# Kernel optimization log

Hardware: AMD Instinct MI355X
Metric: run time of the kernel (lower is better)

Reference implementation:

```python
import jax, jax.numpy as jnp
import numpy as np

N = 40000    # nodes
E = 500000   # edges
B = 512      # graphs
NEG_SLOPE = 0.2


def setup_inputs() -> dict:
    key = jax.random.key(0)
    ks = jax.random.split(key, 32)
    p = lambda i, shape: jax.random.normal(ks[i], shape, jnp.float32) * 0.1
    return dict(
        x=jax.random.normal(ks[0], (N, 4), jnp.float32),
        edge_index=jax.random.randint(ks[1], (2, E), 0, N),
        edge_attr=jax.random.normal(ks[2], (E, 1), jnp.float32),
        batch=jnp.sort(jax.random.randint(ks[3], (N,), 0, B)),
        w0=p(4, (1, 4)), b0=p(5, (4,)),
        wl1=p(6, (7, 256)), wr1=p(7, (7, 256)), we1=p(8, (1, 256)), att1=p(9, (8, 32)), b1=p(10, (256,)),
        wl2=p(11, (256, 128)), wr2=p(12, (256, 128)), we2=p(13, (1, 128)), att2=p(14, (8, 16)), b2=p(15, (128,)),
        wl3=p(16, (128, 8)), wr3=p(17, (128, 8)), we3=p(18, (1, 8)), att3=p(19, (1, 8)), b3=p(20, (8,)),
        w4=p(21, (8, 1)), b4=p(22, (1,)),
    )


def _gatv2(x, src, dst, ea, wl, wr, we, att, bias, heads, ch):
    # GATv2Conv: score = att . leaky_relu(Wl x_src + Wr x_dst + We e), segment softmax over dst
    n = x.shape[0]
    xl = (x @ wl).reshape(n, heads, ch)      # source transform [n,H,C]
    xr = (x @ wr).reshape(n, heads, ch)      # target transform
    ee = (ea @ we).reshape(-1, heads, ch)    # edge transform   [Ef,H,C]
    s = jax.nn.leaky_relu(xl[src] + xr[dst] + ee, NEG_SLOPE)
    logits = jnp.einsum('ehc,hc->eh', s, att)
    m = jax.lax.stop_gradient(jax.ops.segment_max(logits, dst, num_segments=n))
    ex = jnp.exp(logits - m[dst])
    denom = jax.ops.segment_sum(ex, dst, num_segments=n)
    alpha = ex / denom[dst]                  # softmax over incoming edges of each node
    out = jax.ops.segment_sum(alpha[:, :, None] * xl[src], dst, num_segments=n)
    return out.reshape(n, heads * ch) + bias


def _forward(x, edge_index, edge_attr, batch,
             w0, b0, wl1, wr1, we1, att1, b1, wl2, wr2, we2, att2, b2,
             wl3, wr3, we3, att3, b3, w4, b4):
    src, dst = edge_index[0], edge_index[1]
    n = x.shape[0]
    # add self loops (PyG default, fill_value='mean' = mean of incoming edge_attr)
    deg = jax.ops.segment_sum(jnp.ones((src.shape[0],), jnp.float32), dst, num_segments=n)
    esum = jax.ops.segment_sum(edge_attr, dst, num_segments=n)
    loop_attr = jnp.where(deg[:, None] > 0, esum / jnp.maximum(deg, 1.0)[:, None], 0.0)
    idx = jnp.arange(n)
    src_f = jnp.concatenate([src, idx])
    dst_f = jnp.concatenate([dst, idx])
    ea_f = jnp.concatenate([edge_attr, loop_attr], axis=0)
    # embed atom type, keep xyz -> 7 features
    h = jnp.concatenate([x[:, :1] @ w0 + b0, x[:, 1:]], axis=1)
    h = jnp.tanh(_gatv2(h, src_f, dst_f, ea_f, wl1, wr1, we1, att1, b1, 8, 32))
    # dropout(p=0.6) is identity in eval mode
    h = jnp.tanh(_gatv2(h, src_f, dst_f, ea_f, wl2, wr2, we2, att2, b2, 8, 16))
    h = jnp.tanh(_gatv2(h, src_f, dst_f, ea_f, wl3, wr3, we3, att3, b3, 1, 8))
    # scatter-mean pooling per graph
    cnt = jax.ops.segment_sum(jnp.ones((n,), jnp.float32), batch, num_segments=B)
    pooled = jax.ops.segment_sum(h, batch, num_segments=B) / jnp.maximum(cnt, 1.0)[:, None]
    return pooled @ w4 + b4  # [B,1]


def reference(x, edge_index, edge_attr, batch, w0, b0, wl1, wr1, we1, att1, b1,
              wl2, wr2, we2, att2, b2, wl3, wr3, we3, att3, b3, w4, b4):
    return _forward(x, edge_index, edge_attr, batch, w0, b0, wl1, wr1, we1, att1, b1,
                    wl2, wr2, we2, att2, b2, wl3, wr3, we3, att3, b3, w4, b4)
```

## Files before the change

kernel.cpp:

```cpp
#include <hip/hip_runtime.h>
#include <math.h>

#define NN 40000
#define NNP 40064
#define NE 500000
#define NEF (NN + NE)
#define NB 512
#define NEG 0.2f

static inline int cdiv(int a, int b) { return (a + b - 1) / b; }

typedef __attribute__((ext_vector_type(8))) short short8;
typedef __attribute__((ext_vector_type(4))) short short4v;
typedef __attribute__((ext_vector_type(4))) float f32x4;
typedef __attribute__((ext_vector_type(2))) _Float16 half2v;

__device__ __forceinline__ unsigned short f2bf(float f) {
  unsigned u = __float_as_uint(f);
  unsigned r = (u + 0x7fffu + ((u >> 16) & 1u)) >> 16;
  return (unsigned short)r;
}
__device__ __forceinline__ float bf2f(unsigned short h) {
  return __uint_as_float((unsigned)h << 16);
}
__device__ __forceinline__ float lrelu(float v) {
  return fmaxf(v, NEG * v);
}
__device__ __forceinline__ float red8(float p) {
  p += __uint_as_float((unsigned)__builtin_amdgcn_mov_dpp((int)__float_as_uint(p), 0xB1, 0xF, 0xF, true));
  p += __uint_as_float((unsigned)__builtin_amdgcn_mov_dpp((int)__float_as_uint(p), 0x4E, 0xF, 0xF, true));
  p += __uint_as_float((unsigned)__builtin_amdgcn_mov_dpp((int)__float_as_uint(p), 0x141, 0xF, 0xF, true));
  return p;
}

__global__ void k_deg(const int* __restrict__ ei, const float* __restrict__ ea,
                      int* __restrict__ degi, float* __restrict__ esum) {
  int e = blockIdx.x * 256 + threadIdx.x;
  if (e < NE) {
    int d = ei[NE + e];
    atomicAdd(degi + d, 1);
    atomicAdd(esum + d, ea[e]);
  }
}

__global__ void k_scanA(const int* __restrict__ degi, int* __restrict__ pre,
                        int* __restrict__ bsum, float* __restrict__ lpa) {
  __shared__ int sh[256];
  int t = threadIdx.x, i = blockIdx.x * 256 + t;
  int dg = i < NN ? degi[i] : -1;
  sh[t] = i < NN ? dg + 1 : 0;
  if (i < NN) lpa[i] = dg > 0 ? lpa[i] / (float)dg : 0.f;
  __syncthreads();
  for (int st = 1; st < 256; st <<= 1) {
    int a = t >= st ? sh[t - st] : 0;
    __syncthreads();
    sh[t] += a;
    __syncthreads();
  }
  if (i < NN) pre[i] = sh[t];
  if (t == 255) bsum[blockIdx.x] = sh[255];
}

__global__ void k_scan2(int* __restrict__ bsum, int nb) {
  __shared__ int sh[256];
  int t = threadIdx.x;
  sh[t] = t < nb ? bsum[t] : 0;
  __syncthreads();
  for (int st = 1; st < 256; st <<= 1) {
    int a = t >= st ? sh[t - st] : 0;
    __syncthreads();
    sh[t] += a;
    __syncthreads();
  }
  if (t < nb) bsum[t] = sh[t];
}

__global__ void k_scan3(const int* __restrict__ pre, const int* __restrict__ bsum,
                        int* __restrict__ rowptr) {
  int i = blockIdx.x * 256 + threadIdx.x;
  if (i < NN) {
    int off = blockIdx.x > 0 ? bsum[blockIdx.x - 1] : 0;
    rowptr[i + 1] = pre[i] + off;
    if (i == 0) rowptr[0] = 0;
  }
}

__global__ void k_fill(const int* __restrict__ ei, const float* __restrict__ ea,
                       const float* __restrict__ lpa, const int* __restrict__ rowptr,
                       int* __restrict__ fillc, int* __restrict__ csrc,
                       float* __restrict__ ceav) {
  int e = blockIdx.x * 256 + threadIdx.x;
  if (e >= NEF) return;
  int s, d;
  float v;
  if (e < NE) { s = ei[e]; d = ei[NE + e]; v = ea[e]; }
  else        { s = e - NE; d = s; v = lpa[s]; }
  int pos = atomicAdd(fillc + d, 1);
  int idx = rowptr[d] + pos;
  csrc[idx] = s;
  ceav[idx] = v;
}

__global__ __launch_bounds__(256) void k_gat1(const int* __restrict__ rowptr,
                                              const int* __restrict__ csrc,
                                              const float* __restrict__ ceav,
                                              const float* __restrict__ xx,
                                              const float* __restrict__ w0,
                                              const float* __restrict__ b0,
                                              const float* __restrict__ wl,
                                              const float* __restrict__ wr,
                                              const float* __restrict__ we,
                                              const float* __restrict__ att,
                                              const float* __restrict__ bias,
                                              short* __restrict__ ah,
                                              short* __restrict__ al) {
  const int lane = threadIdx.x & 63;
  const int node = __builtin_amdgcn_readfirstlane(blockIdx.x * 4 + (threadIdx.x >> 6));
  const int j0 = lane * 4;
  if (node >= NN) {
    short4v z = {0, 0, 0, 0};
    *(short4v*)(ah + (size_t)node * 256 + j0) = z;
    *(short4v*)(al + (size_t)node * 256 + j0) = z;
    return;
  }

  float4 wev = *(const float4*)(we + j0);
  float4 attv = *(const float4*)(att + j0);
  float w0s[4] = {w0[0], w0[1], w0[2], w0[3]};
  float b0s[4] = {b0[0], b0[1], b0[2], b0[3]};
  float u[4] = {0.f, 0.f, 0.f, 0.f}, v[4] = {0.f, 0.f, 0.f, 0.f};
#pragma unroll
  for (int j = 0; j < 4; j++) {
    float4 t = *(const float4*)(wl + j * 256 + j0);
    float tt[4] = {t.x, t.y, t.z, t.w};
#pragma unroll
    for (int c = 0; c < 4; c++) {
      u[c] = fmaf(w0s[j], tt[c], u[c]);
      v[c] = fmaf(b0s[j], tt[c], v[c]);
    }
  }
  float4 wl4 = *(const float4*)(wl + 4 * 256 + j0);
  float4 wl5 = *(const float4*)(wl + 5 * 256 + j0);
  float4 wl6 = *(const float4*)(wl + 6 * 256 + j0);

  float xrr[4] = {0.f, 0.f, 0.f, 0.f};
  {
    float4 xv = *(const float4*)(xx + (size_t)node * 4);
    float hn[7] = {fmaf(xv.x, w0s[0], b0s[0]), fmaf(xv.x, w0s[1], b0s[1]),
                   fmaf(xv.x, w0s[2], b0s[2]), fmaf(xv.x, w0s[3], b0s[3]),
                   xv.y, xv.z, xv.w};
#pragma unroll
    for (int k = 0; k < 7; k++) {
      float4 t = *(const float4*)(wr + k * 256 + j0);
      xrr[0] = fmaf(hn[k], t.x, xrr[0]);
      xrr[1] = fmaf(hn[k], t.y, xrr[1]);
      xrr[2] = fmaf(hn[k], t.z, xrr[2]);
      xrr[3] = fmaf(hn[k], t.w, xrr[3]);
    }
  }

  float m = -INFINITY, den = 0.f;
  float acc[4] = {0.f, 0.f, 0.f, 0.f};
  const int kb = rowptr[node], ke = rowptr[node + 1];
  int s = csrc[kb];
  float eav = ceav[kb];
  float4 xs = *(const float4*)(xx + (size_t)s * 4);
  for (int k = kb; k < ke; k++) {
    const int idx = (k + 1 < ke) ? k + 1 : k;
    const int s2 = csrc[idx];
    const float eav2 = ceav[idx];
    const float4 xs2 = *(const float4*)(xx + (size_t)s2 * 4);

    float xls[4];
#pragma unroll
    for (int c = 0; c < 4; c++) xls[c] = fmaf(xs.x, u[c], v[c]);
    xls[0] = fmaf(xs.y, wl4.x, xls[0]); xls[1] = fmaf(xs.y, wl4.y, xls[1]);
    xls[2] = fmaf(xs.y, wl4.z, xls[2]); xls[3] = fmaf(xs.y, wl4.w, xls[3]);
    xls[0] = fmaf(xs.z, wl5.x, xls[0]); xls[1] = fmaf(xs.z, wl5.y, xls[1]);
    xls[2] = fmaf(xs.z, wl5.z, xls[2]); xls[3] = fmaf(xs.z, wl5.w, xls[3]);
    xls[0] = fmaf(xs.w, wl6.x, xls[0]); xls[1] = fmaf(xs.w, wl6.y, xls[1]);
    xls[2] = fmaf(xs.w, wl6.z, xls[2]); xls[3] = fmaf(xs.w, wl6.w, xls[3]);

    float p = 0.f;
    p = fmaf(lrelu(xls[0] + fmaf(eav, wev.x, xrr[0])), attv.x, p);
    p = fmaf(lrelu(xls[1] + fmaf(eav, wev.y, xrr[1])), attv.y, p);
    p = fmaf(lrelu(xls[2] + fmaf(eav, wev.z, xrr[2])), attv.z, p);
    p = fmaf(lrelu(xls[3] + fmaf(eav, wev.w, xrr[3])), attv.w, p);
    p = red8(p);
    if (!__all(p <= m + 8.f)) {
      float mn = fmaxf(m, p);
      float sc = __expf(m - mn);
      den *= sc;
#pragma unroll
      for (int c = 0; c < 4; c++) acc[c] *= sc;
      m = mn;
    }
    float ex = __expf(p - m);
    den += ex;
#pragma unroll
    for (int c = 0; c < 4; c++) acc[c] = fmaf(ex, xls[c], acc[c]);
    s = s2; eav = eav2; xs = xs2;
  }
  float rd = 1.f / den;
  float4 bv = *(const float4*)(bias + j0);
  float bb[4] = {bv.x, bv.y, bv.z, bv.w};
  short hi[4], lo[4];
#pragma unroll
  for (int c = 0; c < 4; c++) {
    float hv = tanhf(fmaf(acc[c], rd, bb[c]));
    unsigned short hb = f2bf(hv);
    hi[c] = (short)hb;
    lo[c] = (short)f2bf(hv - bf2f(hb));
  }
  *(short4v*)(ah + (size_t)node * 256 + j0) = *(short4v*)hi;
  *(short4v*)(al + (size_t)node * 256 + j0) = *(short4v*)lo;
}

__global__ void k_wsplit(const float* __restrict__ wl, const float* __restrict__ wr,
                         short* __restrict__ bh, short* __restrict__ bl) {
  int id = blockIdx.x * 256 + threadIdx.x;
  int n = id >> 8, k = id & 255;
  float w = n < 128 ? wl[k * 128 + n] : wr[k * 128 + n - 128];
  unsigned short hb = f2bf(w);
  bh[n * 256 + k] = (short)hb;
  bl[n * 256 + k] = (short)f2bf(w - bf2f(hb));
}

__global__ __launch_bounds__(256) void k_gemm2(const short* __restrict__ ah,
                                               const short* __restrict__ al,
                                               const short* __restrict__ bh,
                                               const short* __restrict__ bl,
                                               _Float16* __restrict__ xlh,
                                               float* __restrict__ xr) {
  __shared__ short sAh[128 * 40];
  __shared__ short sAl[128 * 40];
  __shared__ short sBh[64 * 40];
  __shared__ short sBl[64 * 40];
  const int tid = threadIdx.x;
  const int bm = blockIdx.x >> 2, bn = blockIdx.x & 3;
  const int wid = tid >> 6, lane = tid & 63;
  const int wr = wid >> 1, wc = wid & 1;
  const int l15 = lane & 15, lhi = lane >> 4;
  const int srow = tid >> 2;
  const int kq = (tid & 3) * 8;
  f32x4 acc[4][2];
#pragma unroll
  for (int a = 0; a < 4; a++)
#pragma unroll
    for (int b = 0; b < 2; b++) acc[a][b] = (f32x4)(0.f);

#pragma unroll 1
  for (int st = 0; st < 8; st++) {
    const int k0 = st * 32;
    const long aoff0 = (long)(bm * 128 + srow) * 256 + k0 + kq;
    const long aoff1 = aoff0 + 64 * 256;
    const long boff = (long)(bn * 64 + srow) * 256 + k0 + kq;
    short8 vah0 = *(const short8*)(ah + aoff0);
    short8 vah1 = *(const short8*)(ah + aoff1);
    short8 val0 = *(const short8*)(al + aoff0);
    short8 val1 = *(const short8*)(al + aoff1);
    short8 vbh  = *(const short8*)(bh + boff);
    short8 vbl  = *(const short8*)(bl + boff);
    __syncthreads();
    *(short8*)&sAh[srow * 40 + kq] = vah0;
    *(short8*)&sAh[(64 + srow) * 40 + kq] = vah1;
    *(short8*)&sAl[srow * 40 + kq] = val0;
    *(short8*)&sAl[(64 + srow) * 40 + kq] = val1;
    *(short8*)&sBh[srow * 40 + kq] = vbh;
    *(short8*)&sBl[srow * 40 + kq] = vbl;
    __syncthreads();
    short8 bfh[2], bfl[2];
#pragma unroll
    for (int fn = 0; fn < 2; fn++) {
      bfh[fn] = *(const short8*)&sBh[(wc * 32 + fn * 16 + l15) * 40 + lhi * 8];
      bfl[fn] = *(const short8*)&sBl[(wc * 32 + fn * 16 + l15) * 40 + lhi * 8];
    }
#pragma unroll
    for (int fm = 0; fm < 4; fm++) {
      short8 afh = *(const short8*)&sAh[(wr * 64 + fm * 16 + l15) * 40 + lhi * 8];
      short8 afl = *(const short8*)&sAl[(wr * 64 + fm * 16 + l15) * 40 + lhi * 8];
      acc[fm][0] = __builtin_amdgcn_mfma_f32_16x16x32_bf16(afh, bfh[0], acc[fm][0], 0, 0, 0);
      acc[fm][1] = __builtin_amdgcn_mfma_f32_16x16x32_bf16(afh, bfh[1], acc[fm][1], 0, 0, 0);
      acc[fm][0] = __builtin_amdgcn_mfma_f32_16x16x32_bf16(afh, bfl[0], acc[fm][0], 0, 0, 0);
      acc[fm][1] = __builtin_amdgcn_mfma_f32_16x16x32_bf16(afh, bfl[1], acc[fm][1], 0, 0, 0);
      acc[fm][0] = __builtin_amdgcn_mfma_f32_16x16x32_bf16(afl, bfh[0], acc[fm][0], 0, 0, 0);
      acc[fm][1] = __builtin_amdgcn_mfma_f32_16x16x32_bf16(afl, bfh[1], acc[fm][1], 0, 0, 0);
    }
  }
#pragma unroll
  for (int fm = 0; fm < 4; fm++)
#pragma unroll
    for (int fn = 0; fn < 2; fn++) {
      int col = bn * 64 + wc * 32 + fn * 16 + l15;
#pragma unroll
      for (int j = 0; j < 4; j++) {
        int row = bm * 128 + wr * 64 + fm * 16 + lhi * 4 + j;
        if (col < 128) xlh[(long)row * 128 + col] = (_Float16)acc[fm][fn][j];
        else           xr[(long)row * 128 + col - 128] = acc[fm][fn][j];
      }
    }
}

__global__ __launch_bounds__(256) void k_gat2(const int* __restrict__ rowptr,
                                              const int* __restrict__ csrc,
                                              const float* __restrict__ ceav,
                                              const _Float16* __restrict__ xlh,
                                              const float* __restrict__ xr,
                                              const float* __restrict__ we,
                                              const float* __restrict__ att,
                                              const float* __restrict__ bias,
                                              float* __restrict__ hout) {
  const int lane = threadIdx.x & 63;
  const int node = __builtin_amdgcn_readfirstlane(blockIdx.x * 4 + (threadIdx.x >> 6));
  if (node >= NN) return;
  const int j0 = lane * 2;
  float2 xrr = *(const float2*)(xr + (long)node * 128 + j0);
  float2 wev = *(const float2*)(we + j0);
  float2 attv = *(const float2*)(att + j0);
  float m = -INFINITY, den = 0.f, acc0 = 0.f, acc1 = 0.f;
  const int kb = rowptr[node], ke = rowptr[node + 1];
  int s = csrc[kb];
  float eav = ceav[kb];
  half2v a = *(const half2v*)(xlh + (long)s * 128 + j0);
  for (int k = kb; k < ke; k++) {
    const int idx = (k + 1 < ke) ? k + 1 : k;
    const int s2 = csrc[idx];
    const float eav2 = ceav[idx];
    const half2v a2 = *(const half2v*)(xlh + (long)s2 * 128 + j0);
    float av0 = (float)a.x, av1 = (float)a.y;
    float v0 = lrelu(av0 + fmaf(eav, wev.x, xrr.x));
    float v1 = lrelu(av1 + fmaf(eav, wev.y, xrr.y));
    float p = red8(fmaf(v0, attv.x, v1 * attv.y));
    if (!__all(p <= m + 8.f)) {
      float mn = fmaxf(m, p);
      float sc = __expf(m - mn);
      den *= sc;
      acc0 *= sc;
      acc1 *= sc;
      m = mn;
    }
    float ex = __expf(p - m);
    den += ex;
    acc0 = fmaf(ex, av0, acc0);
    acc1 = fmaf(ex, av1, acc1);
    s = s2; eav = eav2; a = a2;
  }
  float rd = 1.f / den;
  hout[(long)node * 128 + j0]     = tanhf(fmaf(acc0, rd, bias[j0]));
  hout[(long)node * 128 + j0 + 1] = tanhf(fmaf(acc1, rd, bias[j0 + 1]));
}

__global__ __launch_bounds__(256) void k_mm3(const float* __restrict__ h,
                                             const float* __restrict__ wl,
                                             const float* __restrict__ wr,
                                             float* __restrict__ xl,
                                             float* __restrict__ xr) {
  __shared__ float srow[64 * 132];
  __shared__ float lw[128 * 16];
  const int t = threadIdx.x;
  const int n0 = blockIdx.x * 64;
#pragma unroll
  for (int q = 0; q < 8; q++) {
    int gi = (t + q * 256) * 4;
    int row = gi >> 7, col = gi & 127;
    float4 v = *(const float4*)(h + (size_t)(n0 + row) * 128 + col);
    *(float4*)&srow[row * 132 + col] = v;
  }
#pragma unroll
  for (int q = 0; q < 8; q++) {
    int idx = t + q * 256;
    int k = idx >> 4, j = idx & 15;
    lw[idx] = j < 8 ? wl[k * 8 + j] : wr[k * 8 + (j - 8)];
  }
  __syncthreads();
  const int nid = t >> 2, g = t & 3;
  float a0 = 0.f, a1 = 0.f, a2 = 0.f, a3 = 0.f;
  const float* rp = &srow[nid * 132];
  for (int k = 0; k < 128; k++) {
    float hv = rp[k];
    float4 w = *(const float4*)&lw[k * 16 + g * 4];
    a0 = fmaf(hv, w.x, a0);
    a1 = fmaf(hv, w.y, a1);
    a2 = fmaf(hv, w.z, a2);
    a3 = fmaf(hv, w.w, a3);
  }
  float4 r = {a0, a1, a2, a3};
  int node = n0 + nid;
  float* dst = (g & 2) ? xr : xl;
  *(float4*)(dst + node * 8 + (g & 1) * 4) = r;
}

__global__ __launch_bounds__(256) void k_gat3(const int* __restrict__ rowptr,
                                              const int* __restrict__ csrc,
                                              const float* __restrict__ ceav,
                                              const float* __restrict__ xl,
                                              const float* __restrict__ xr,
                                              const float* __restrict__ we,
                                              const float* __restrict__ att,
                                              const float* __restrict__ bias,
                                              float* __restrict__ hout) {
  const int lane = threadIdx.x & 7;
  const int node = blockIdx.x * 32 + (threadIdx.x >> 3);
  if (node >= NN) return;
  const float xrr = xr[node * 8 + lane];
  const float wev = we[lane];
  const float attv = att[lane];
  float m = -INFINITY, den = 0.f, acc = 0.f;
  const int kb = rowptr[node], ke = rowptr[node + 1];
  for (int k = kb; k < ke; k++) {
    const int s = csrc[k];
    const float eav = ceav[k];
    const float av = xl[s * 8 + lane];
    float v = lrelu(av + fmaf(eav, wev, xrr));
    float p = red8(v * attv);
    if (p > m + 8.f) {
      float mn = fmaxf(m, p);
      float sc = __expf(m - mn);
      den *= sc;
      acc *= sc;
      m = mn;
    }
    float ex = __expf(p - m);
    den += ex;
    acc = fmaf(ex, av, acc);
  }
  hout[node * 8 + lane] = tanhf(acc / den + bias[lane]);
}

__global__ void k_gbound(const int* __restrict__ bat, int* __restrict__ gstart) {
  int i = blockIdx.x * 256 + threadIdx.x;
  if (i >= NN) return;
  int b = bat[i];
  int bp = i > 0 ? bat[i - 1] : -1;
  for (int g = bp + 1; g <= b; g++) gstart[g] = i;
  if (i == NN - 1)
    for (int g = b + 1; g <= NB; g++) gstart[g] = NN;
}

__global__ __launch_bounds__(256) void k_poolG(const int* __restrict__ gstart,
                                               const float* __restrict__ h3,
                                               const float* __restrict__ w4,
                                               const float* __restrict__ b4,
                                               float* __restrict__ out) {
  const int lane = threadIdx.x & 63;
  const int g = blockIdx.x * 4 + (threadIdx.x >> 6);
  if (g >= NB) return;
  const int kb = gstart[g], ke = gstart[g + 1];
  const int ch = lane & 7, no = lane >> 3;
  float acc = 0.f;
  for (int n = kb + no; n < ke; n += 8)
    acc += h3[(size_t)n * 8 + ch];
  acc += __shfl_xor(acc, 8);
  acc += __shfl_xor(acc, 16);
  acc += __shfl_xor(acc, 32);
  float cnt = fmaxf((float)(ke - kb), 1.f);
  float yv = (acc / cnt) * w4[ch];
  yv = red8(yv);
  if (lane == 0) out[g] = yv + b4[0];
}

extern "C" void kernel_launch(void* const* d_in, const int* in_sizes, int n_in,
                              void* d_out, int out_size, void* d_ws, size_t ws_size,
                              hipStream_t stream) {
  const float* x   = (const float*)d_in[0];
  const int*   ei  = (const int*)d_in[1];
  const float* ea  = (const float*)d_in[2];
  const int*   bat = (const int*)d_in[3];
  const float* w0  = (const float*)d_in[4];
  const float* b0  = (const float*)d_in[5];
  const float* wl1 = (const float*)d_in[6];
  const float* wr1 = (const float*)d_in[7];
  const float* we1 = (const float*)d_in[8];
  const float* at1 = (const float*)d_in[9];
  const float* b1  = (const float*)d_in[10];
  const float* wl2 = (const float*)d_in[11];
  const float* wr2 = (const float*)d_in[12];
  const float* we2 = (const float*)d_in[13];
  const float* at2 = (const float*)d_in[14];
  const float* b2  = (const float*)d_in[15];
  const float* wl3 = (const float*)d_in[16];
  const float* wr3 = (const float*)d_in[17];
  const float* we3 = (const float*)d_in[18];
  const float* at3 = (const float*)d_in[19];
  const float* b3  = (const float*)d_in[20];
  const float* w4  = (const float*)d_in[21];
  const float* b4  = (const float*)d_in[22];
  float* out = (float*)d_out;

  char* W = (char*)d_ws;
  size_t o = 0;
  auto alloc = [&](size_t bytes) { void* p = W + o; o += (bytes + 255) & ~(size_t)255; return p; };
  int*      degi   = (int*)alloc(NN * 4);
  int*      fillc  = (int*)alloc(NN * 4);
  float*    lpa    = (float*)alloc(NN * 4);
  int*      rowptr = (int*)alloc((NN + 1) * 4);
  int*      pre    = (int*)alloc(NN * 4);
  int*      bsum   = (int*)alloc(256 * 4);
  int*      gstart = (int*)alloc((NB + 1) * 4);
  int*      csrc   = (int*)alloc((size_t)NEF * 4);
  float*    ceav   = (float*)alloc((size_t)NEF * 4);
  short*    Ah     = (short*)alloc((size_t)NNP * 256 * 2);
  short*    Al     = (short*)alloc((size_t)NNP * 256 * 2);
  short*    Bh     = (short*)alloc((size_t)256 * 256 * 2);
  short*    Bl     = (short*)alloc((size_t)256 * 256 * 2);
  _Float16* Xlh2   = (_Float16*)alloc((size_t)NNP * 128 * 2);
  float*    Xr2    = (float*)alloc((size_t)NNP * 128 * 4);
  float*    H2     = (float*)alloc((size_t)NN * 128 * 4);
  float*    Xl3    = (float*)alloc((size_t)NN * 8 * 4);
  float*    Xr3    = (float*)alloc((size_t)NN * 8 * 4);
  float*    H3     = (float*)alloc((size_t)NN * 8 * 4);
  (void)ws_size; (void)in_sizes; (void)n_in; (void)out_size;

  const int NBLK = cdiv(NN, 256);

  hipMemsetAsync(degi, 0, 3 * NN * 4, stream);
  k_deg<<<cdiv(NE, 256), 256, 0, stream>>>(ei, ea, degi, lpa);
  k_scanA<<<NBLK, 256, 0, stream>>>(degi, pre, bsum, lpa);
  k_scan2<<<1, 256, 0, stream>>>(bsum, NBLK);
  k_scan3<<<NBLK, 256, 0, stream>>>(pre, bsum, rowptr);
  k_fill<<<cdiv(NEF, 256), 256, 0, stream>>>(ei, ea, lpa, rowptr, fillc, csrc, ceav);
  k_gbound<<<NBLK, 256, 0, stream>>>(bat, gstart);

  k_gat1<<<NNP / 4, 256, 0, stream>>>(rowptr, csrc, ceav, x, w0, b0, wl1, wr1, we1, at1, b1, Ah, Al);

  k_wsplit<<<256, 256, 0, stream>>>(wl2, wr2, Bh, Bl);
  k_gemm2<<<(NNP / 128) * 4, 256, 0, stream>>>(Ah, Al, Bh, Bl, Xlh2, Xr2);
  k_gat2<<<cdiv(NN, 4), 256, 0, stream>>>(rowptr, csrc, ceav, Xlh2, Xr2, we2, at2, b2, H2);

  k_mm3<<<NN / 64, 256, 0, stream>>>(H2, wl3, wr3, Xl3, Xr3);
  k_gat3<<<cdiv(NN, 32), 256, 0, stream>>>(rowptr, csrc, ceav, Xl3, Xr3, we3, at3, b3, H3);

  k_poolG<<<cdiv(NB, 4), 256, 0, stream>>>(gstart, H3, w4, b4, out);
}
```

Measured before the change: 256.5 us.

## Prefetch two edges ahead in GAT gathers and enlarge GEMM2 M tile

The edge loops in the layer-1 and layer-2 attention kernels now process two edges per iteration and prefetch the next two source rows and edge attributes. This keeps more gather loads in flight to hide memory latency. Separately, the layer-2 split-bf16 GEMM tile grows from 128 to 256 rows per block, with more accumulators per wave, to reuse the B tile more. Node padding is raised to a multiple of 256 to match. The cost is higher register and LDS use and fewer GEMM blocks, which may lower occupancy.

```diff
diff --git a/kernel.cpp b/kernel.cpp
--- a/kernel.cpp
+++ b/kernel.cpp
@@ -2,7 +2,7 @@
 #include <math.h>
 
 #define NN 40000
-#define NNP 40064
+#define NNP 40192
 #define NE 500000
 #define NEF (NN + NE)
 #define NB 512
@@ -162,45 +162,56 @@
   float m = -INFINITY, den = 0.f;
   float acc[4] = {0.f, 0.f, 0.f, 0.f};
   const int kb = rowptr[node], ke = rowptr[node + 1];
-  int s = csrc[kb];
-  float eav = ceav[kb];
-  float4 xs = *(const float4*)(xx + (size_t)s * 4);
-  for (int k = kb; k < ke; k++) {
-    const int idx = (k + 1 < ke) ? k + 1 : k;
-    const int s2 = csrc[idx];
-    const float eav2 = ceav[idx];
-    const float4 xs2 = *(const float4*)(xx + (size_t)s2 * 4);
-
-    float xls[4];
-#pragma unroll
-    for (int c = 0; c < 4; c++) xls[c] = fmaf(xs.x, u[c], v[c]);
-    xls[0] = fmaf(xs.y, wl4.x, xls[0]); xls[1] = fmaf(xs.y, wl4.y, xls[1]);
-    xls[2] = fmaf(xs.y, wl4.z, xls[2]); xls[3] = fmaf(xs.y, wl4.w, xls[3]);
-    xls[0] = fmaf(xs.z, wl5.x, xls[0]); xls[1] = fmaf(xs.z, wl5.y, xls[1]);
-    xls[2] = fmaf(xs.z, wl5.z, xls[2]); xls[3] = fmaf(xs.z, wl5.w, xls[3]);
-    xls[0] = fmaf(xs.w, wl6.x, xls[0]); xls[1] = fmaf(xs.w, wl6.y, xls[1]);
-    xls[2] = fmaf(xs.w, wl6.z, xls[2]); xls[3] = fmaf(xs.w, wl6.w, xls[3]);
-
-    float p = 0.f;
-    p = fmaf(lrelu(xls[0] + fmaf(eav, wev.x, xrr[0])), attv.x, p);
-    p = fmaf(lrelu(xls[1] + fmaf(eav, wev.y, xrr[1])), attv.y, p);
-    p = fmaf(lrelu(xls[2] + fmaf(eav, wev.z, xrr[2])), attv.z, p);
-    p = fmaf(lrelu(xls[3] + fmaf(eav, wev.w, xrr[3])), attv.w, p);
-    p = red8(p);
-    if (!__all(p <= m + 8.f)) {
-      float mn = fmaxf(m, p);
-      float sc = __expf(m - mn);
-      den *= sc;
-#pragma unroll
-      for (int c = 0; c < 4; c++) acc[c] *= sc;
-      m = mn;
-    }
-    float ex = __expf(p - m);
-    den += ex;
-#pragma unroll
-    for (int c = 0; c < 4; c++) acc[c] = fmaf(ex, xls[c], acc[c]);
-    s = s2; eav = eav2; xs = xs2;
-  }
+
+#define G1_EDGE(XS, EAV)                                                        \
+  {                                                                             \
+    float xls[4];                                                               \
+    _Pragma("unroll")                                                           \
+    for (int c = 0; c < 4; c++) xls[c] = fmaf((XS).x, u[c], v[c]);              \
+    xls[0] = fmaf((XS).y, wl4.x, xls[0]); xls[1] = fmaf((XS).y, wl4.y, xls[1]); \
+    xls[2] = fmaf((XS).y, wl4.z, xls[2]); xls[3] = fmaf((XS).y, wl4.w, xls[3]); \
+    xls[0] = fmaf((XS).z, wl5.x, xls[0]); xls[1] = fmaf((XS).z, wl5.y, xls[1]); \
+    xls[2] = fmaf((XS).z, wl5.z, xls[2]); xls[3] = fmaf((XS).z, wl5.w, xls[3]); \
+    xls[0] = fmaf((XS).w, wl6.x, xls[0]); xls[1] = fmaf((XS).w, wl6.y, xls[1]); \
+    xls[2] = fmaf((XS).w, wl6.z, xls[2]); xls[3] = fmaf((XS).w, wl6.w, xls[3]); \
+    float p = 0.f;                                                              \
+    p = fmaf(lrelu(xls[0] + fmaf((EAV), wev.x, xrr[0])), attv.x, p);            \
+    p = fmaf(lrelu(xls[1] + fmaf((EAV), wev.y, xrr[1])), attv.y, p);            \
+    p = fmaf(lrelu(xls[2] + fmaf((EAV), wev.z, xrr[2])), attv.z, p);            \
+    p = fmaf(lrelu(xls[3] + fmaf((EAV), wev.w, xrr[3])), attv.w, p);            \
+    p = red8(p);                                                                \
+    if (!__all(p <= m + 8.f)) {                                                 \
+      float mn = fmaxf(m, p);                                                   \
+      float sc = __expf(m - mn);                                                \
+      den *= sc;                                                                \
+      _Pragma("unroll")                                                         \
+      for (int c = 0; c < 4; c++) acc[c] *= sc;                                 \
+      m = mn;                                                                   \
+    }                                                                           \
+    float ex = __expf(p - m);                                                   \
+    den += ex;                                                                  \
+    _Pragma("unroll")                                                           \
+    for (int c = 0; c < 4; c++) acc[c] = fmaf(ex, xls[c], acc[c]);              \
+  }
+
+  int i1 = kb + 1 < ke ? kb + 1 : ke - 1;
+  float eA = ceav[kb], eB = ceav[i1];
+  float4 xA = *(const float4*)(xx + (size_t)csrc[kb] * 4);
+  float4 xB = *(const float4*)(xx + (size_t)csrc[i1] * 4);
+  for (int k = kb; k < ke; k += 2) {
+    const int i2 = k + 2 < ke ? k + 2 : ke - 1;
+    const int i3 = k + 3 < ke ? k + 3 : ke - 1;
+    const float eC = ceav[i2], eD = ceav[i3];
+    const float4 xC = *(const float4*)(xx + (size_t)csrc[i2] * 4);
+    const float4 xD = *(const float4*)(xx + (size_t)csrc[i3] * 4);
+    G1_EDGE(xA, eA);
+    if (k + 1 < ke) {
+      G1_EDGE(xB, eB);
+    }
+    xA = xC; eA = eC; xB = xD; eB = eD;
+  }
+#undef G1_EDGE
+
   float rd = 1.f / den;
   float4 bv = *(const float4*)(bias + j0);
   float bb[4] = {bv.x, bv.y, bv.z, bv.w};
@@ -232,8 +243,8 @@
                                                const short* __restrict__ bl,
                                                _Float16* __restrict__ xlh,
                                                float* __restrict__ xr) {
-  __shared__ short sAh[128 * 40];
-  __shared__ short sAl[128 * 40];
+  __shared__ short sAh[256 * 40];
+  __shared__ short sAl[256 * 40];
   __shared__ short sBh[64 * 40];
   __shared__ short sBl[64 * 40];
   const int tid = threadIdx.x;
@@ -243,29 +254,33 @@
   const int l15 = lane & 15, lhi = lane >> 4;
   const int srow = tid >> 2;
   const int kq = (tid & 3) * 8;
-  f32x4 acc[4][2];
-#pragma unroll
-  for (int a = 0; a < 4; a++)
+  f32x4 acc[8][2];
+#pragma unroll
+  for (int a = 0; a < 8; a++)
 #pragma unroll
     for (int b = 0; b < 2; b++) acc[a][b] = (f32x4)(0.f);
 
 #pragma unroll 1
   for (int st = 0; st < 8; st++) {
     const int k0 = st * 32;
-    const long aoff0 = (long)(bm * 128 + srow) * 256 + k0 + kq;
-    const long aoff1 = aoff0 + 64 * 256;
-    const long boff = (long)(bn * 64 + srow) * 256 + k0 + kq;
-    short8 vah0 = *(const short8*)(ah + aoff0);
-    short8 vah1 = *(const short8*)(ah + aoff1);
-    short8 val0 = *(const short8*)(al + aoff0);
-    short8 val1 = *(const short8*)(al + aoff1);
-    short8 vbh  = *(const short8*)(bh + boff);
-    short8 vbl  = *(const short8*)(bl + boff);
+    short8 vh[4], vl[4], vbh, vbl;
+#pragma unroll
+    for (int ps = 0; ps < 4; ps++) {
+      const long off = (long)(bm * 256 + ps * 64 + srow) * 256 + k0 + kq;
+      vh[ps] = *(const short8*)(ah + off);
+      vl[ps] = *(const short8*)(al + off);
+    }
+    {
+      const long boff = (long)(bn * 64 + srow) * 256 + k0 + kq;
+      vbh = *(const short8*)(bh + boff);
+      vbl = *(const short8*)(bl + boff);
+    }
     __syncthreads();
-    *(short8*)&sAh[srow * 40 + kq] = vah0;
-    *(short8*)&sAh[(64 + srow) * 40 + kq] = vah1;
-    *(short8*)&sAl[srow * 40 + kq] = val0;
-    *(short8*)&sAl[(64 + srow) * 40 + kq] = val1;
+#pragma unroll
+    for (int ps = 0; ps < 4; ps++) {
+      *(short8*)&sAh[(ps * 64 + srow) * 40 + kq] = vh[ps];
+      *(short8*)&sAl[(ps * 64 + srow) * 40 + kq] = vl[ps];
+    }
     *(short8*)&sBh[srow * 40 + kq] = vbh;
     *(short8*)&sBl[srow * 40 + kq] = vbl;
     __syncthreads();
@@ -276,9 +291,9 @@
       bfl[fn] = *(const short8*)&sBl[(wc * 32 + fn * 16 + l15) * 40 + lhi * 8];
     }
 #pragma unroll
-    for (int fm = 0; fm < 4; fm++) {
-      short8 afh = *(const short8*)&sAh[(wr * 64 + fm * 16 + l15) * 40 + lhi * 8];
-      short8 afl = *(const short8*)&sAl[(wr * 64 + fm * 16 + l15) * 40 + lhi * 8];
+    for (int fm = 0; fm < 8; fm++) {
+      short8 afh = *(const short8*)&sAh[(wr * 128 + fm * 16 + l15) * 40 + lhi * 8];
+      short8 afl = *(const short8*)&sAl[(wr * 128 + fm * 16 + l15) * 40 + lhi * 8];
       acc[fm][0] = __builtin_amdgcn_mfma_f32_16x16x32_bf16(afh, bfh[0], acc[fm][0], 0, 0, 0);
       acc[fm][1] = __builtin_amdgcn_mfma_f32_16x16x32_bf16(afh, bfh[1], acc[fm][1], 0, 0, 0);
       acc[fm][0] = __builtin_amdgcn_mfma_f32_16x16x32_bf16(afh, bfl[0], acc[fm][0], 0, 0, 0);
@@ -288,13 +303,13 @@
     }
   }
 #pragma unroll
-  for (int fm = 0; fm < 4; fm++)
+  for (int fm = 0; fm < 8; fm++)
 #pragma unroll
     for (int fn = 0; fn < 2; fn++) {
       int col = bn * 64 + wc * 32 + fn * 16 + l15;
 #pragma unroll
       for (int j = 0; j < 4; j++) {
-        int row = bm * 128 + wr * 64 + fm * 16 + lhi * 4 + j;
+        int row = bm * 256 + wr * 128 + fm * 16 + lhi * 4 + j;
         if (col < 128) xlh[(long)row * 128 + col] = (_Float16)acc[fm][fn][j];
         else           xr[(long)row * 128 + col - 128] = acc[fm][fn][j];
       }
@@ -319,32 +334,45 @@
   float2 attv = *(const float2*)(att + j0);
   float m = -INFINITY, den = 0.f, acc0 = 0.f, acc1 = 0.f;
   const int kb = rowptr[node], ke = rowptr[node + 1];
-  int s = csrc[kb];
-  float eav = ceav[kb];
-  half2v a = *(const half2v*)(xlh + (long)s * 128 + j0);
-  for (int k = kb; k < ke; k++) {
-    const int idx = (k + 1 < ke) ? k + 1 : k;
-    const int s2 = csrc[idx];
-    const float eav2 = ceav[idx];
-    const half2v a2 = *(const half2v*)(xlh + (long)s2 * 128 + j0);
-    float av0 = (float)a.x, av1 = (float)a.y;
-    float v0 = lrelu(av0 + fmaf(eav, wev.x, xrr.x));
-    float v1 = lrelu(av1 + fmaf(eav, wev.y, xrr.y));
-    float p = red8(fmaf(v0, attv.x, v1 * attv.y));
-    if (!__all(p <= m + 8.f)) {
-      float mn = fmaxf(m, p);
-      float sc = __expf(m - mn);
-      den *= sc;
-      acc0 *= sc;
-      acc1 *= sc;
-      m = mn;
-    }
-    float ex = __expf(p - m);
-    den += ex;
-    acc0 = fmaf(ex, av0, acc0);
-    acc1 = fmaf(ex, av1, acc1);
-    s = s2; eav = eav2; a = a2;
-  }
+
+#define G2_EDGE(AV, EAV)                                                  \
+  {                                                                       \
+    float av0 = (float)(AV).x, av1 = (float)(AV).y;                       \
+    float v0 = lrelu(av0 + fmaf((EAV), wev.x, xrr.x));                    \
+    float v1 = lrelu(av1 + fmaf((EAV), wev.y, xrr.y));                    \
+    float p = red8(fmaf(v0, attv.x, v1 * attv.y));                        \
+    if (!__all(p <= m + 8.f)) {                                           \
+      float mn = fmaxf(m, p);                                             \
+      float sc = __expf(m - mn);                                          \
+      den *= sc;                                                          \
+      acc0 *= sc;                                                         \
+      acc1 *= sc;                                                         \
+      m = mn;                                                             \
+    }                                                                     \
+    float ex = __expf(p - m);                                             \
+    den += ex;                                                            \
+    acc0 = fmaf(ex, av0, acc0);                                           \
+    acc1 = fmaf(ex, av1, acc1);                                           \
+  }
+
+  int i1 = kb + 1 < ke ? kb + 1 : ke - 1;
+  float eA = ceav[kb], eB = ceav[i1];
+  half2v aA = *(const half2v*)(xlh + (long)csrc[kb] * 128 + j0);
+  half2v aB = *(const half2v*)(xlh + (long)csrc[i1] * 128 + j0);
+  for (int k = kb; k < ke; k += 2) {
+    const int i2 = k + 2 < ke ? k + 2 : ke - 1;
+    const int i3 = k + 3 < ke ? k + 3 : ke - 1;
+    const float eC = ceav[i2], eD = ceav[i3];
+    const half2v aC = *(const half2v*)(xlh + (long)csrc[i2] * 128 + j0);
+    const half2v aD = *(const half2v*)(xlh + (long)csrc[i3] * 128 + j0);
+    G2_EDGE(aA, eA);
+    if (k + 1 < ke) {
+      G2_EDGE(aB, eB);
+    }
+    aA = aC; eA = eC; aB = aD; eB = eD;
+  }
+#undef G2_EDGE
+
   float rd = 1.f / den;
   hout[(long)node * 128 + j0]     = tanhf(fmaf(acc0, rd, bias[j0]));
   hout[(long)node * 128 + j0 + 1] = tanhf(fmaf(acc1, rd, bias[j0 + 1]));
@@ -524,7 +552,7 @@
   k_gat1<<<NNP / 4, 256, 0, stream>>>(rowptr, csrc, ceav, x, w0, b0, wl1, wr1, we1, at1, b1, Ah, Al);
 
   k_wsplit<<<256, 256, 0, stream>>>(wl2, wr2, Bh, Bl);
-  k_gemm2<<<(NNP / 128) * 4, 256, 0, stream>>>(Ah, Al, Bh, Bl, Xlh2, Xr2);
+  k_gemm2<<<(NNP / 256) * 4, 256, 0, stream>>>(Ah, Al, Bh, Bl, Xlh2, Xr2);
   k_gat2<<<cdiv(NN, 4), 256, 0, stream>>>(rowptr, csrc, ceav, Xlh2, Xr2, we2, at2, b2, H2);
 
   k_mm3<<<NN / 64, 256, 0, stream>>>(H2, wl3, wr3, Xl3, Xr3);
```

Measured after the change: 260.0 us. No clear change (+1.4%).
